# Kernel tuning notes

Measured on AMD Instinct MI355X. Metric: run time of the kernel, lower is better.

Reference implementation:

```python
import jax, jax.numpy as jnp
import numpy as np
from jax import lax

# Dimensions (must match input_specs)
B, T, C = 2, 2048, 1024
H = 4 * C          # FFN hidden
E_RWKV, E_TRANS = 6, 2
E = E_RWKV + E_TRANS
LN_EPS = 1e-5


def layernorm(x, g, b):
    m = x.mean(-1, keepdims=True)
    v = ((x - m) ** 2).mean(-1, keepdims=True)
    return (x - m) * lax.rsqrt(v + LN_EPS) * g + b


def setup_inputs() -> dict:
    key = jax.random.key(0)
    ks = jax.random.split(key, 24)
    s = 0.02
    inp = {
        "x": jax.random.normal(ks[0], (B, T, C), jnp.float32),
        "v_first": jax.random.normal(ks[1], (B, T, C), jnp.float32),
        "winners": jax.random.randint(ks[2], (B, T, 2), 0, E),
        "capital_shares": jax.random.uniform(ks[3], (E,), jnp.float32),
        # LayerNorms
        "ln1_g": jnp.ones((C,), jnp.float32), "ln1_b": jnp.zeros((C,), jnp.float32),
        "ln2_g": jnp.ones((C,), jnp.float32), "ln2_b": jnp.zeros((C,), jnp.float32),
        # RWKV-style time-mix (simplified RWKV7_TimeMix)
        "Wr": s * jax.random.normal(ks[4], (C, C), jnp.float32),
        "Wk": s * jax.random.normal(ks[5], (C, C), jnp.float32),
        "Wv": s * jax.random.normal(ks[6], (C, C), jnp.float32),
        "Wo": s * jax.random.normal(ks[7], (C, C), jnp.float32),
        "w_decay": jax.random.normal(ks[8], (C,), jnp.float32),
        "g_v": jax.random.normal(ks[9], (C,), jnp.float32),
        # bridge: linear on concat(h, rwkv_state)
        "Wb": s * jax.random.normal(ks[10], (2 * C, C), jnp.float32),
        "bb": jnp.zeros((C,), jnp.float32),
        # 6 stacked SparseRWKVFFN experts: sigmoid(x Wr_r) * (relu(x Wk_r)^2 Wv_r)
        "Wk_r": s * jax.random.normal(ks[11], (E_RWKV, C, H), jnp.float32),
        "Wv_r": s * jax.random.normal(ks[12], (E_RWKV, H, C), jnp.float32),
        "Wr_r": s * jax.random.normal(ks[13], (E_RWKV, C, C), jnp.float32),
        # 2 stacked LinearTransformerExpert: gelu((h+prefix) W1) W2
        "W1_t": s * jax.random.normal(ks[14], (E_TRANS, C, H), jnp.float32),
        "W2_t": s * jax.random.normal(ks[15], (E_TRANS, H, C), jnp.float32),
    }
    return inp


def reference(x, v_first, winners, capital_shares,
              ln1_g, ln1_b, ln2_g, ln2_b,
              Wr, Wk, Wv, Wo, w_decay, g_v,
              Wb, bb, Wk_r, Wv_r, Wr_r, W1_t, W2_t):
    # ---- attention (simplified RWKV time-mix), returns per-token state ----
    h1 = layernorm(x, ln1_g, ln1_b)
    r = jax.nn.sigmoid(h1 @ Wr)                      # [B,T,C]
    k = h1 @ Wk
    v = h1 @ Wv
    v = v + (v_first - v) * jax.nn.sigmoid(g_v)      # value-residual mix
    w = jax.nn.sigmoid(w_decay)                      # per-channel decay [C]

    def step(s, kv):
        k_t, v_t = kv                                # [B,C] each
        s = w * s + k_t * v_t
        return s, s

    s0 = jnp.zeros((B, C), x.dtype)
    _, states = lax.scan(step, s0, (jnp.swapaxes(k, 0, 1), jnp.swapaxes(v, 0, 1)))
    states = jnp.swapaxes(states, 0, 1)              # rwkv_state [B,T,C]

    att_out = (r * states) @ Wo
    x = x + att_out
    h = layernorm(x, ln2_g, ln2_b)

    # ---- bridge prefix (flat over tokens, vectorized) ----
    bridge_prefix = jnp.concatenate([h, states], axis=-1) @ Wb + bb  # [B,T,C]

    # ---- experts computed densely, combined by top-2 gates ----
    # RWKV FFN experts
    a = jnp.square(jax.nn.relu(jnp.einsum('btc,ech->ebth', h, Wk_r)))     # [Er,B,T,H]
    rec = jax.nn.sigmoid(jnp.einsum('btc,ecd->ebtd', h, Wr_r))            # [Er,B,T,C]
    out_r = rec * jnp.einsum('ebth,ehc->ebtc', a, Wv_r)                   # [Er,B,T,C]
    # Linear-transformer experts consume the bridge prefix
    ht = h + bridge_prefix
    out_t = jnp.einsum('ebth,ehc->ebtc',
                       jax.nn.gelu(jnp.einsum('btc,ech->ebth', ht, W1_t)),
                       W2_t)                                              # [Et,B,T,C]
    all_out = jnp.concatenate([out_r, out_t], axis=0)                     # [E,B,T,C]

    # top-2 combine, each rank weighted 0.5 (use_market=False branch)
    gate = 0.5 * (jax.nn.one_hot(winners[..., 0], E, dtype=x.dtype)
                  + jax.nn.one_hot(winners[..., 1], E, dtype=x.dtype))    # [B,T,E]
    final_out = jnp.einsum('ebtc,bte->btc', all_out, gate)

    return x + final_out
```

## Files before the change

### kernel.cpp

```cpp
#include <hip/hip_runtime.h>

typedef unsigned short u16;
typedef __bf16 bf16x8 __attribute__((ext_vector_type(8)));
typedef float f32x4 __attribute__((ext_vector_type(4)));

__device__ __forceinline__ float bf2f(u16 u){ union{unsigned i;float f;}x; x.i=((unsigned)u)<<16; return x.f; }
__device__ __forceinline__ u16 f2bf(float f){ union{float f;unsigned i;}x; x.f=f; unsigned r = x.i + 0x7FFFu + ((x.i>>16)&1u); return (u16)(r>>16); }
__device__ __forceinline__ float sigm(float x){ return 1.f/(1.f+expf(-x)); }

struct __align__(8) U16x4 { u16 v[4]; };

#define PSTRIDE 8388608ull

struct CJob { const float* src; u16* dst; int K, N, base; };
struct CJobs { CJob j[27]; };

__global__ void conv_all(CJobs cj){
  __shared__ u16 tile[128][65];
  int id = blockIdx.x;
  int sel = 0;
  #pragma unroll
  for (int i=1;i<27;++i) if (cj.j[i].base <= id) sel = i;
  const float* __restrict__ src = cj.j[sel].src;
  u16* __restrict__ dst = cj.j[sel].dst;
  int K = cj.j[sel].K, N = cj.j[sel].N;
  int lt = id - cj.j[sel].base;
  int tn = N >> 6;
  int k0 = (lt / tn) * 128, n0 = (lt % tn) * 64;
  int tid = threadIdx.x;
  #pragma unroll
  for (int it=0; it<8; ++it){
    int e = it*1024 + tid*4;
    int r = e>>6, c = e&63;
    float4 v = *(const float4*)(src + (size_t)(k0+r)*N + n0 + c);
    tile[r][c+0]=f2bf(v.x); tile[r][c+1]=f2bf(v.y); tile[r][c+2]=f2bf(v.z); tile[r][c+3]=f2bf(v.w);
  }
  __syncthreads();
  #pragma unroll
  for (int it=0; it<8; ++it){
    int e = it*1024 + tid*4;
    int n = e>>7, k = e&127;
    U16x4 o;
    #pragma unroll
    for (int j=0;j<4;++j) o.v[j] = tile[k+j][n];
    *(U16x4*)(dst + (size_t)(n0+n)*K + k0 + k) = o;
  }
}

__global__ void ln_k(const float* __restrict__ x, const float* __restrict__ g, const float* __restrict__ b,
                     u16* __restrict__ out, int ostride){
  int row = blockIdx.x, tid = threadIdx.x;
  float4 v = *(const float4*)(x + (size_t)row*1024 + tid*4);
  float s = v.x+v.y+v.z+v.w;
  float ss = v.x*v.x+v.y*v.y+v.z*v.z+v.w*v.w;
  #pragma unroll
  for (int o=32;o;o>>=1){ s += __shfl_down(s,o); ss += __shfl_down(ss,o); }
  __shared__ float sm[8];
  int lane = tid&63, wv = tid>>6;
  if (!lane){ sm[wv]=s; sm[4+wv]=ss; }
  __syncthreads();
  s = sm[0]+sm[1]+sm[2]+sm[3]; ss = sm[4]+sm[5]+sm[6]+sm[7];
  float mean = s*(1.f/1024.f);
  float var = ss*(1.f/1024.f) - mean*mean;
  float inv = rsqrtf(var + 1e-5f);
  U16x4 o;
  const float* vp = &v.x;
  #pragma unroll
  for (int j=0;j<4;++j){
    int c = tid*4+j;
    o.v[j] = f2bf((vp[j]-mean)*inv*g[c] + b[c]);
  }
  *(U16x4*)(out + (size_t)row*ostride + tid*4) = o;
}

__global__ void red_x_ln(const float* __restrict__ x, const u16* __restrict__ part,
                         const float* __restrict__ g, const float* __restrict__ b,
                         float* __restrict__ out, u16* __restrict__ hcat){
  int row = blockIdx.x, tid = threadIdx.x;
  size_t i = (size_t)row*1024 + tid*4;
  U16x4 p0 = *(const U16x4*)(part + i);
  U16x4 p1 = *(const U16x4*)(part + PSTRIDE + i);
  float4 xv = *(const float4*)(x + i);
  float4 v;
  v.x = xv.x + bf2f(p0.v[0]) + bf2f(p1.v[0]);
  v.y = xv.y + bf2f(p0.v[1]) + bf2f(p1.v[1]);
  v.z = xv.z + bf2f(p0.v[2]) + bf2f(p1.v[2]);
  v.w = xv.w + bf2f(p0.v[3]) + bf2f(p1.v[3]);
  *(float4*)(out + i) = v;
  float s = v.x+v.y+v.z+v.w;
  float ss = v.x*v.x+v.y*v.y+v.z*v.z+v.w*v.w;
  #pragma unroll
  for (int o=32;o;o>>=1){ s += __shfl_down(s,o); ss += __shfl_down(ss,o); }
  __shared__ float sm[8];
  int lane = tid&63, wv = tid>>6;
  if (!lane){ sm[wv]=s; sm[4+wv]=ss; }
  __syncthreads();
  s = sm[0]+sm[1]+sm[2]+sm[3]; ss = sm[4]+sm[5]+sm[6]+sm[7];
  float mean = s*(1.f/1024.f);
  float var = ss*(1.f/1024.f) - mean*mean;
  float inv = rsqrtf(var + 1e-5f);
  U16x4 o;
  const float* vp = &v.x;
  #pragma unroll
  for (int j=0;j<4;++j){
    int c = tid*4+j;
    o.v[j] = f2bf((vp[j]-mean)*inv*g[c] + b[c]);
  }
  *(U16x4*)(hcat + (size_t)row*2048 + tid*4) = o;
}

__global__ void scan_p1(const u16* __restrict__ kbuf, const u16* __restrict__ vbuf,
                        const float* __restrict__ w_decay, float* __restrict__ carry){
  int c = blockIdx.x*256 + threadIdx.x;
  int chunk = blockIdx.y, b = blockIdx.z;
  float w = sigm(w_decay[c]);
  float s = 0.f;
  size_t idx = ((size_t)(b*2048 + chunk*64))*1024 + c;
  #pragma unroll 4
  for (int i=0;i<64;++i){ s = w*s + bf2f(kbuf[idx])*bf2f(vbuf[idx]); idx += 1024; }
  carry[((size_t)(b*32+chunk))*1024 + c] = s;
}
__global__ void scan_p2(const float* __restrict__ w_decay, const float* __restrict__ carry,
                        float* __restrict__ startv){
  int c = blockIdx.x*256 + threadIdx.x;
  int b = blockIdx.y;
  float w = sigm(w_decay[c]);
  float wL = w;
  #pragma unroll
  for (int i=0;i<6;++i) wL *= wL;
  float p = 0.f;
  for (int j=0;j<32;++j){
    size_t id = ((size_t)(b*32+j))*1024 + c;
    startv[id] = p;
    p = wL*p + carry[id];
  }
}
__global__ void scan_p3(const u16* __restrict__ kbuf, const u16* __restrict__ vbuf, const u16* __restrict__ rbuf,
                        const float* __restrict__ w_decay, const float* __restrict__ startv,
                        u16* __restrict__ rs, u16* __restrict__ hcat){
  int c = blockIdx.x*256 + threadIdx.x;
  int chunk = blockIdx.y, b = blockIdx.z;
  float w = sigm(w_decay[c]);
  float s = startv[((size_t)(b*32+chunk))*1024 + c];
  size_t t0 = (size_t)b*2048 + chunk*64;
  size_t idx = t0*1024 + c;
  size_t idx2 = t0*2048 + 1024 + c;
  for (int i=0;i<64;++i){
    s = w*s + bf2f(kbuf[idx])*bf2f(vbuf[idx]);
    rs[idx] = f2bf(bf2f(rbuf[idx]) * s);
    hcat[idx2] = f2bf(s);
    idx += 1024; idx2 += 2048;
  }
}

__global__ void route_count(const int* __restrict__ winners, int* __restrict__ offs, int* __restrict__ cursor){
  __shared__ int cnt[8];
  if (threadIdx.x < 8) cnt[threadIdx.x] = 0;
  __syncthreads();
  for (int p = threadIdx.x; p < 8192; p += 256) atomicAdd(&cnt[winners[p]&7], 1);
  __syncthreads();
  if (threadIdx.x == 0){
    int s = 0;
    #pragma unroll
    for (int e=0;e<8;++e){ offs[e]=s; s+=cnt[e]; }
    offs[8]=s;
  }
  if (threadIdx.x < 8) cursor[threadIdx.x] = 0;
}
__global__ void route_scatter(const int* __restrict__ winners, const int* __restrict__ offs,
                              int* __restrict__ cursor, int* __restrict__ idx_all){
  int p = blockIdx.x*256 + threadIdx.x;
  if (p < 8192){
    int e = winners[p]&7;
    int pos = offs[e] + atomicAdd(&cursor[e], 1);
    idx_all[pos] = p>>1;
  }
}

struct GArgs {
  const u16* A; const u16* B;
  long long lda, bstride;
  int K, Mdense, eBase, nxt, kdiv;
  const int* offs; const int* idx_all;
  const float* v_first; const float* g_v;
  u16* rbuf; u16* kbuf; u16* vbuf;
  u16* act; u16* part;
};

#define GLL(gp, lp) __builtin_amdgcn_global_load_lds((const __attribute__((address_space(1))) void*)(gp), \
                                                     (__attribute__((address_space(3))) void*)(lp), 16, 0, 0)

template<int EPI, int GATHER>
__global__ __launch_bounds__(256,3) void gemm_k(GArgs g){
  int e = g.eBase + blockIdx.z;
  int rbase = 0, m = g.Mdense;
  if (g.offs){ rbase = g.offs[e]; m = g.offs[e+1] - rbase; }
  if ((int)blockIdx.y * 128 >= m) return;
  const int xt = (int)blockIdx.x % g.nxt;
  const int ksplit = (int)blockIdx.x / g.nxt;
  const long long kOff = (long long)ksplit * g.kdiv;
  __shared__ char smem[49152];
  const int tid = threadIdx.x, lane = tid&63, wave = tid>>6;
  const int wr = wave>>1, wc = wave&1;
  const int nk = g.kdiv >> 5;

  const int srowi = tid>>2;
  const long long scol = (long long)((tid&3)*8);

  const u16* bBase0 = g.B + (long long)blockIdx.z*g.bstride
                    + ((long long)(xt*128) + srowi)*(long long)g.K + kOff + scol;
  const u16* bBase1 = bBase0 + 64ll*(long long)g.K;

  int aRd[4], bRd[4];
  #pragma unroll
  for (int q=0;q<4;++q){
    aRd[q] = (wr*64 + q*16 + (lane&15))*64 + (lane>>4)*16;
    bRd[q] = 8192 + (wc*64 + q*16 + (lane&15))*64 + (lane>>4)*16;
  }

  for (int mt = blockIdx.y; mt*128 < m; mt += gridDim.y){
    const u16 *aP0, *aP1;
    {
      int g0 = mt*128 + srowi;       g0 = g0 < m ? g0 : m-1;
      int g1 = mt*128 + 64 + srowi;  g1 = g1 < m ? g1 : m-1;
      long long r0, r1;
      if (GATHER){ r0 = g.idx_all[rbase+g0]; r1 = g.idx_all[rbase+g1]; }
      else if (g.offs){ r0 = rbase+g0; r1 = rbase+g1; }
      else { r0 = g0; r1 = g1; }
      aP0 = g.A + r0*g.lda + kOff + scol;
      aP1 = g.A + r1*g.lda + kOff + scol;
    }
    const u16* bP0 = bBase0;
    const u16* bP1 = bBase1;

    f32x4 acc[4][4];
    #pragma unroll
    for (int mm=0;mm<4;++mm)
      #pragma unroll
      for (int nn=0;nn<4;++nn)
        acc[mm][nn] = f32x4{0.f,0.f,0.f,0.f};

    #define STAGE(BUF) do{ \
      char* db = smem + (BUF)*16384 + wave*1024; \
      GLL(aP0, db); GLL(aP1, db+4096); GLL(bP0, db+8192); GLL(bP1, db+12288); \
      aP0+=32; aP1+=32; bP0+=32; bP1+=32; }while(0)

    STAGE(0); STAGE(1);
    int bufC = 0, bufS = 2;
    for (int ks=0; ks<nk; ++ks){
      if (ks+2 < nk){
        STAGE(bufS); bufS = bufS==2 ? 0 : bufS+1;
        asm volatile("s_waitcnt vmcnt(8)" ::: "memory");
      } else if (ks+1 < nk){
        asm volatile("s_waitcnt vmcnt(4)" ::: "memory");
      } else {
        asm volatile("s_waitcnt vmcnt(0)" ::: "memory");
      }
      asm volatile("s_barrier" ::: "memory");
      const char* base = smem + bufC*16384;
      bf16x8 af[4], bfv[4];
      #pragma unroll
      for (int q=0;q<4;++q) af[q] = *(const bf16x8*)(base + aRd[q]);
      #pragma unroll
      for (int q=0;q<4;++q) bfv[q] = *(const bf16x8*)(base + bRd[q]);
      #pragma unroll
      for (int mm=0;mm<4;++mm)
        #pragma unroll
        for (int nn=0;nn<4;++nn)
          acc[mm][nn] = __builtin_amdgcn_mfma_f32_16x16x32_bf16(af[mm], bfv[nn], acc[mm][nn], 0,0,0);
      asm volatile("s_waitcnt lgkmcnt(0)" ::: "memory");
      asm volatile("s_barrier" ::: "memory");
      bufC = bufC==2 ? 0 : bufC+1;
    }
    #undef STAGE

    int colB = xt*128 + wc*64 + (lane&15);
    #pragma unroll
    for (int mm=0;mm<4;++mm){
      #pragma unroll
      for (int j=0;j<4;++j){
        int grow = mt*128 + wr*64 + mm*16 + (lane>>4)*4 + j;
        if (grow >= m) continue;
        size_t gr = (size_t)(rbase + grow);
        #pragma unroll
        for (int nn=0;nn<4;++nn){
          int col = colB + nn*16;
          float val = acc[mm][nn][j];
          if (EPI==0){
            if (col < 1024) g.rbuf[gr*1024+col] = f2bf(sigm(val));
            else if (col < 2048) g.kbuf[gr*1024+col-1024] = f2bf(val);
            else {
              int c2 = col-2048;
              float sg = sigm(g.g_v[c2]);
              float vf = g.v_first[gr*1024+c2];
              g.vbuf[gr*1024+c2] = f2bf(val + (vf-val)*sg);
            }
          } else {
            g.part[(size_t)ksplit*PSTRIDE + gr*1024 + col] = f2bf(val);
          }
        }
      }
    }
  }
}

struct MoeArgs {
  const u16* hcat; const u16* htb; const u16* act;
  const u16* wTkr; const u16* wT1; const u16* wTrr; const u16* wTvr; const u16* wT2;
  const int* offs; const int* idx_all;
  u16* actw; u16* part;
};

template<int PHASE>
__global__ __launch_bounds__(256,3) void gemm_moe(MoeArgs g){
  int z = blockIdx.z;
  const u16 *Ap, *Bp; long long lda; int K, kdiv, nxt, e, epi;
  if (PHASE==0){
    if (z < 6){ e=z;   Ap=g.hcat; lda=2048; Bp=g.wTkr + (long long)z*4096*1024;     K=1024; kdiv=1024; nxt=32; epi=0; }
    else if (z < 8){ e=z; Ap=g.htb; lda=1024; Bp=g.wT1 + (long long)(z-6)*4096*1024; K=1024; kdiv=1024; nxt=32; epi=1; }
    else { e=z-8; Ap=g.hcat; lda=2048; Bp=g.wTrr + (long long)(z-8)*1024*1024;      K=1024; kdiv=512;  nxt=8;  epi=2; }
  } else {
    if (z < 6){ e=z; Ap=g.act; lda=4096; Bp=g.wTvr + (long long)z*1024*4096;        K=4096; kdiv=2048; nxt=8;  epi=3; }
    else { e=z;     Ap=g.act; lda=4096; Bp=g.wT2 + (long long)(z-6)*1024*4096;      K=4096; kdiv=1024; nxt=8;  epi=4; }
  }
  if ((int)blockIdx.x >= nxt * (K / kdiv)) return;
  int rbase = g.offs[e], m = g.offs[e+1] - rbase;
  if ((int)blockIdx.y * 128 >= m) return;
  const int xt = (int)blockIdx.x % nxt;
  const int ksplit = (int)blockIdx.x / nxt;
  const long long kOff = (long long)ksplit * kdiv;
  __shared__ char smem[49152];
  const int tid = threadIdx.x, lane = tid&63, wave = tid>>6;
  const int wr = wave>>1, wc = wave&1;
  const int nk = kdiv >> 5;

  const int srowi = tid>>2;
  const long long scol = (long long)((tid&3)*8);

  const u16* bBase0 = Bp + ((long long)(xt*128) + srowi)*(long long)K + kOff + scol;
  const u16* bBase1 = bBase0 + 64ll*(long long)K;

  int aRd[4], bRd[4];
  #pragma unroll
  for (int q=0;q<4;++q){
    aRd[q] = (wr*64 + q*16 + (lane&15))*64 + (lane>>4)*16;
    bRd[q] = 8192 + (wc*64 + q*16 + (lane&15))*64 + (lane>>4)*16;
  }

  for (int mt = blockIdx.y; mt*128 < m; mt += gridDim.y){
    const u16 *aP0, *aP1;
    {
      int g0 = mt*128 + srowi;       g0 = g0 < m ? g0 : m-1;
      int g1 = mt*128 + 64 + srowi;  g1 = g1 < m ? g1 : m-1;
      long long r0, r1;
      if (epi <= 2){ r0 = g.idx_all[rbase+g0]; r1 = g.idx_all[rbase+g1]; }
      else { r0 = rbase+g0; r1 = rbase+g1; }
      aP0 = Ap + r0*lda + kOff + scol;
      aP1 = Ap + r1*lda + kOff + scol;
    }
    const u16* bP0 = bBase0;
    const u16* bP1 = bBase1;

    f32x4 acc[4][4];
    #pragma unroll
    for (int mm=0;mm<4;++mm)
      #pragma unroll
      for (int nn=0;nn<4;++nn)
        acc[mm][nn] = f32x4{0.f,0.f,0.f,0.f};

    #define STAGE(BUF) do{ \
      char* db = smem + (BUF)*16384 + wave*1024; \
      GLL(aP0, db); GLL(aP1, db+4096); GLL(bP0, db+8192); GLL(bP1, db+12288); \
      aP0+=32; aP1+=32; bP0+=32; bP1+=32; }while(0)

    STAGE(0); STAGE(1);
    int bufC = 0, bufS = 2;
    for (int ks=0; ks<nk; ++ks){
      if (ks+2 < nk){
        STAGE(bufS); bufS = bufS==2 ? 0 : bufS+1;
        asm volatile("s_waitcnt vmcnt(8)" ::: "memory");
      } else if (ks+1 < nk){
        asm volatile("s_waitcnt vmcnt(4)" ::: "memory");
      } else {
        asm volatile("s_waitcnt vmcnt(0)" ::: "memory");
      }
      asm volatile("s_barrier" ::: "memory");
      const char* base = smem + bufC*16384;
      bf16x8 af[4], bfv[4];
      #pragma unroll
      for (int q=0;q<4;++q) af[q] = *(const bf16x8*)(base + aRd[q]);
      #pragma unroll
      for (int q=0;q<4;++q) bfv[q] = *(const bf16x8*)(base + bRd[q]);
      #pragma unroll
      for (int mm=0;mm<4;++mm)
        #pragma unroll
        for (int nn=0;nn<4;++nn)
          acc[mm][nn] = __builtin_amdgcn_mfma_f32_16x16x32_bf16(af[mm], bfv[nn], acc[mm][nn], 0,0,0);
      asm volatile("s_waitcnt lgkmcnt(0)" ::: "memory");
      asm volatile("s_barrier" ::: "memory");
      bufC = bufC==2 ? 0 : bufC+1;
    }
    #undef STAGE

    int colB = xt*128 + wc*64 + (lane&15);
    #pragma unroll
    for (int mm=0;mm<4;++mm){
      #pragma unroll
      for (int j=0;j<4;++j){
        int grow = mt*128 + wr*64 + mm*16 + (lane>>4)*4 + j;
        if (grow >= m) continue;
        size_t gr = (size_t)(rbase + grow);
        #pragma unroll
        for (int nn=0;nn<4;++nn){
          int col = colB + nn*16;
          float val = acc[mm][nn][j];
          if (epi == 0){
            float r_ = fmaxf(val, 0.f);
            g.actw[gr*4096+col] = f2bf(r_*r_);
          } else if (epi == 1){
            float t3 = val*val*val;
            float th = tanhf(0.79788456080286535588f*(val + 0.044715f*t3));
            g.actw[gr*4096+col] = f2bf(0.5f*val*(1.f+th));
          } else if (epi == 2){
            g.part[(size_t)(2+ksplit)*PSTRIDE + gr*1024 + col] = f2bf(val);
          } else {
            g.part[(size_t)ksplit*PSTRIDE + gr*1024 + col] = f2bf(val);
          }
        }
      }
    }
  }
}

__global__ void red_ht(const u16* __restrict__ hcat, const u16* __restrict__ part,
                       const float* __restrict__ bb, u16* __restrict__ ht){
  int c = threadIdx.x*4;
  size_t i = (size_t)blockIdx.x*1024 + c;
  U16x4 p0 = *(const U16x4*)(part + i);
  U16x4 p1 = *(const U16x4*)(part + PSTRIDE + i);
  U16x4 hv = *(const U16x4*)(hcat + (size_t)blockIdx.x*2048 + c);
  U16x4 o;
  #pragma unroll
  for (int j=0;j<4;++j) o.v[j] = f2bf(bf2f(hv.v[j]) + bf2f(p0.v[j]) + bf2f(p1.v[j]) + bb[c+j]);
  *(U16x4*)(ht + i) = o;
}
__global__ void red_moe(const int* __restrict__ offs, const int* __restrict__ idx_all,
                        const u16* __restrict__ part, float* __restrict__ out){
  int gr = blockIdx.x;
  if (gr >= offs[8]) return;
  int tok = idx_all[gr];
  bool isr = gr < offs[6];
  int c = threadIdx.x*4;
  size_t i = (size_t)gr*1024 + c;
  U16x4 p0 = *(const U16x4*)(part + i);
  U16x4 p1 = *(const U16x4*)(part + PSTRIDE + i);
  U16x4 p2 = *(const U16x4*)(part + 2*PSTRIDE + i);
  U16x4 p3 = *(const U16x4*)(part + 3*PSTRIDE + i);
  #pragma unroll
  for (int j=0;j<4;++j){
    float v;
    if (isr){
      float rc = sigm(bf2f(p2.v[j]) + bf2f(p3.v[j]));
      v = 0.5f*(bf2f(p0.v[j]) + bf2f(p1.v[j]))*rc;
    } else {
      v = 0.5f*(bf2f(p0.v[j]) + bf2f(p1.v[j]) + bf2f(p2.v[j]) + bf2f(p3.v[j]));
    }
    atomicAdd(&out[(size_t)tok*1024 + c + j], v);
  }
}

extern "C" void kernel_launch(void* const* d_in, const int* in_sizes, int n_in,
                              void* d_out, int out_size, void* d_ws, size_t ws_size,
                              hipStream_t stream) {
  const float* x       = (const float*)d_in[0];
  const float* v_first = (const float*)d_in[1];
  const int*   winners = (const int*)d_in[2];
  const float* ln1_g   = (const float*)d_in[4];
  const float* ln1_b   = (const float*)d_in[5];
  const float* ln2_g   = (const float*)d_in[6];
  const float* ln2_b   = (const float*)d_in[7];
  const float* Wr      = (const float*)d_in[8];
  const float* Wk      = (const float*)d_in[9];
  const float* Wv      = (const float*)d_in[10];
  const float* Wo      = (const float*)d_in[11];
  const float* w_decay = (const float*)d_in[12];
  const float* g_v     = (const float*)d_in[13];
  const float* Wb      = (const float*)d_in[14];
  const float* bb      = (const float*)d_in[15];
  const float* Wk_r    = (const float*)d_in[16];
  const float* Wv_r    = (const float*)d_in[17];
  const float* Wr_r    = (const float*)d_in[18];
  const float* W1_t    = (const float*)d_in[19];
  const float* W2_t    = (const float*)d_in[20];
  float* out = (float*)d_out;

  char* p = (char*)d_ws;
  auto alloc = [&](size_t bytes)->char*{ char* r=p; p += (bytes+255)&~(size_t)255; return r; };
  u16* wTrkv = (u16*)alloc(3072ull*1024*2);
  u16* wTo   = (u16*)alloc(1024ull*1024*2);
  u16* wTb   = (u16*)alloc(1024ull*2048*2);
  u16* wTkr  = (u16*)alloc(6ull*4096*1024*2);
  u16* wTvr  = (u16*)alloc(6ull*1024*4096*2);
  u16* wTrr  = (u16*)alloc(6ull*1024*1024*2);
  u16* wT1   = (u16*)alloc(2ull*4096*1024*2);
  u16* wT2   = (u16*)alloc(2ull*1024*4096*2);
  u16* h1    = (u16*)alloc(4096ull*1024*2);
  u16* rbuf  = (u16*)alloc(4096ull*1024*2);
  u16* kbuf  = (u16*)alloc(4096ull*1024*2);
  u16* vbuf  = (u16*)alloc(4096ull*1024*2);
  u16* rsb   = (u16*)alloc(4096ull*1024*2);
  u16* hcat  = (u16*)alloc(4096ull*2048*2);
  u16* htb   = (u16*)alloc(4096ull*1024*2);
  u16* act   = (u16*)alloc(8192ull*4096*2);
  u16* partial = (u16*)alloc(4ull*8192*1024*2);
  float* carry  = (float*)alloc(2ull*32*1024*4);
  float* startv = (float*)alloc(2ull*32*1024*4);
  int* offs   = (int*)alloc(16*4);
  int* cursor = (int*)alloc(8*4);
  int* idx_all= (int*)alloc(8192*4);

  dim3 B256(256);

  {
    CJobs cj; int base = 0, ji = 0;
    auto add = [&](const float* s, u16* d, int K, int N){
      cj.j[ji++] = CJob{s, d, K, N, base}; base += (K>>7)*(N>>6);
    };
    add(Wr, wTrkv, 1024,1024); add(Wk, wTrkv+1024*1024, 1024,1024);
    add(Wv, wTrkv+2048*1024, 1024,1024); add(Wo, wTo, 1024,1024);
    add(Wb, wTb, 2048,1024);
    for (int e2=0;e2<6;++e2) add(Wk_r + (size_t)e2*1024*4096, wTkr + (size_t)e2*4096*1024, 1024,4096);
    for (int e2=0;e2<6;++e2) add(Wv_r + (size_t)e2*4096*1024, wTvr + (size_t)e2*1024*4096, 4096,1024);
    for (int e2=0;e2<6;++e2) add(Wr_r + (size_t)e2*1024*1024, wTrr + (size_t)e2*1024*1024, 1024,1024);
    for (int e2=0;e2<2;++e2) add(W1_t + (size_t)e2*1024*4096, wT1 + (size_t)e2*4096*1024, 1024,4096);
    for (int e2=0;e2<2;++e2) add(W2_t + (size_t)e2*4096*1024, wT2 + (size_t)e2*1024*4096, 4096,1024);
    conv_all<<<dim3(base,1,1),B256,0,stream>>>(cj);
  }

  route_count<<<1,B256,0,stream>>>(winners, offs, cursor);
  route_scatter<<<32,B256,0,stream>>>(winners, offs, cursor, idx_all);

  ln_k<<<4096,B256,0,stream>>>(x, ln1_g, ln1_b, h1, 1024);

  {
    GArgs ga{}; ga.A=h1; ga.B=wTrkv; ga.lda=1024; ga.K=1024; ga.Mdense=4096; ga.nxt=24; ga.kdiv=1024;
    ga.v_first=v_first; ga.g_v=g_v; ga.rbuf=rbuf; ga.kbuf=kbuf; ga.vbuf=vbuf;
    gemm_k<0,0><<<dim3(24,32,1),B256,0,stream>>>(ga);
  }

  scan_p1<<<dim3(4,32,2),B256,0,stream>>>(kbuf, vbuf, w_decay, carry);
  scan_p2<<<dim3(4,2,1), B256,0,stream>>>(w_decay, carry, startv);
  scan_p3<<<dim3(4,32,2),B256,0,stream>>>(kbuf, vbuf, rbuf, w_decay, startv, rsb, hcat);

  {
    GArgs ga{}; ga.A=rsb; ga.B=wTo; ga.lda=1024; ga.K=1024; ga.Mdense=4096; ga.nxt=8; ga.kdiv=512;
    ga.part=partial;
    gemm_k<1,0><<<dim3(16,32,1),B256,0,stream>>>(ga);
  }
  red_x_ln<<<4096,B256,0,stream>>>(x, partial, ln2_g, ln2_b, out, hcat);

  {
    GArgs ga{}; ga.A=hcat; ga.B=wTb; ga.lda=2048; ga.K=2048; ga.Mdense=4096; ga.nxt=8; ga.kdiv=1024;
    ga.part=partial;
    gemm_k<2,0><<<dim3(16,32,1),B256,0,stream>>>(ga);
  }
  red_ht<<<4096,B256,0,stream>>>(hcat, partial, bb, htb);

  {
    MoeArgs ma{};
    ma.hcat=hcat; ma.htb=htb; ma.act=act;
    ma.wTkr=wTkr; ma.wT1=wT1; ma.wTrr=wTrr; ma.wTvr=wTvr; ma.wT2=wT2;
    ma.offs=offs; ma.idx_all=idx_all; ma.actw=act; ma.part=partial;
    gemm_moe<0><<<dim3(32,6,14),B256,0,stream>>>(ma);
    gemm_moe<1><<<dim3(32,6,8),B256,0,stream>>>(ma);
  }
  red_moe<<<8192,B256,0,stream>>>(offs, idx_all, partial, out);

  (void)in_sizes; (void)n_in; (void)out_size; (void)ws_size;
}
```

Measured before the change: 747.5 us.

## Swizzle LDS tile layout and remap MoE GEMM block order across XCDs

Applies an XOR swizzle to the 16-byte column chunks written into shared memory by global_load_lds and matches it in the per-lane MFMA read offsets, so the reads hit fewer LDS bank conflicts. Both GEMM kernels get this. The MoE GEMM also remaps its linear block id so that the 8 round-robin-dispatched XCD groups each take a contiguous slice of work, which should improve L2 reuse of weights and activations. The swizzle must match exactly between the write and read patterns or the results are wrong. The remap assumes the total block count divides evenly by 8.

```diff
diff --git a/kernel.cpp b/kernel.cpp
--- a/kernel.cpp
+++ b/kernel.cpp
@@ -177,6 +177,7 @@
   }
 }
 
+
 struct GArgs {
   const u16* A; const u16* B;
   long long lda, bstride;
@@ -205,17 +206,18 @@
   const int nk = g.kdiv >> 5;
 
   const int srowi = tid>>2;
-  const long long scol = (long long)((tid&3)*8);
+  const long long scol = (long long)((((tid&3) ^ ((tid>>3)&3)))*8);
 
   const u16* bBase0 = g.B + (long long)blockIdx.z*g.bstride
                     + ((long long)(xt*128) + srowi)*(long long)g.K + kOff + scol;
   const u16* bBase1 = bBase0 + 64ll*(long long)g.K;
 
+  const int sw = ((lane>>4) ^ ((lane>>1)&3)) << 4;
   int aRd[4], bRd[4];
   #pragma unroll
   for (int q=0;q<4;++q){
-    aRd[q] = (wr*64 + q*16 + (lane&15))*64 + (lane>>4)*16;
-    bRd[q] = 8192 + (wc*64 + q*16 + (lane&15))*64 + (lane>>4)*16;
+    aRd[q] = (wr*64 + q*16 + (lane&15))*64 + sw;
+    bRd[q] = 8192 + (wc*64 + q*16 + (lane&15))*64 + sw;
   }
 
   for (int mt = blockIdx.y; mt*128 < m; mt += gridDim.y){
@@ -313,7 +315,14 @@
 
 template<int PHASE>
 __global__ __launch_bounds__(256,3) void gemm_moe(MoeArgs g){
-  int z = blockIdx.z;
+  const int T  = (int)(gridDim.x*gridDim.y*gridDim.z);
+  const int id = (int)(blockIdx.x + gridDim.x*(blockIdx.y + gridDim.y*blockIdx.z));
+  const int work = (id&7)*(T>>3) + (id>>3);
+  const int bx = work % (int)gridDim.x;
+  const int rest = work / (int)gridDim.x;
+  const int by = rest % (int)gridDim.y;
+  const int z  = rest / (int)gridDim.y;
+
   const u16 *Ap, *Bp; long long lda; int K, kdiv, nxt, e, epi;
   if (PHASE==0){
     if (z < 6){ e=z;   Ap=g.hcat; lda=2048; Bp=g.wTkr + (long long)z*4096*1024;     K=1024; kdiv=1024; nxt=32; epi=0; }
@@ -323,11 +332,11 @@
     if (z < 6){ e=z; Ap=g.act; lda=4096; Bp=g.wTvr + (long long)z*1024*4096;        K=4096; kdiv=2048; nxt=8;  epi=3; }
     else { e=z;     Ap=g.act; lda=4096; Bp=g.wT2 + (long long)(z-6)*1024*4096;      K=4096; kdiv=1024; nxt=8;  epi=4; }
   }
-  if ((int)blockIdx.x >= nxt * (K / kdiv)) return;
+  if (bx >= nxt * (K / kdiv)) return;
   int rbase = g.offs[e], m = g.offs[e+1] - rbase;
-  if ((int)blockIdx.y * 128 >= m) return;
-  const int xt = (int)blockIdx.x % nxt;
-  const int ksplit = (int)blockIdx.x / nxt;
+  if (by * 128 >= m) return;
+  const int xt = bx % nxt;
+  const int ksplit = bx / nxt;
   const long long kOff = (long long)ksplit * kdiv;
   __shared__ char smem[49152];
   const int tid = threadIdx.x, lane = tid&63, wave = tid>>6;
@@ -335,19 +344,20 @@
   const int nk = kdiv >> 5;
 
   const int srowi = tid>>2;
-  const long long scol = (long long)((tid&3)*8);
+  const long long scol = (long long)((((tid&3) ^ ((tid>>3)&3)))*8);
 
   const u16* bBase0 = Bp + ((long long)(xt*128) + srowi)*(long long)K + kOff + scol;
   const u16* bBase1 = bBase0 + 64ll*(long long)K;
 
+  const int sw = ((lane>>4) ^ ((lane>>1)&3)) << 4;
   int aRd[4], bRd[4];
   #pragma unroll
   for (int q=0;q<4;++q){
-    aRd[q] = (wr*64 + q*16 + (lane&15))*64 + (lane>>4)*16;
-    bRd[q] = 8192 + (wc*64 + q*16 + (lane&15))*64 + (lane>>4)*16;
-  }
-
-  for (int mt = blockIdx.y; mt*128 < m; mt += gridDim.y){
+    aRd[q] = (wr*64 + q*16 + (lane&15))*64 + sw;
+    bRd[q] = 8192 + (wc*64 + q*16 + (lane&15))*64 + sw;
+  }
+
+  for (int mt = by; mt*128 < m; mt += gridDim.y){
     const u16 *aP0, *aP1;
     {
       int g0 = mt*128 + srowi;       g0 = g0 < m ? g0 : m-1;
```

Result: faster. 712.6 us (-4.7%).
